# Optimization experiments

Hardware: AMD Instinct MI355X
Metric: run time of the kernel (lower is better)

The kernel has to match this reference:

```python
import jax, jax.numpy as jnp
import numpy as np

B, CIN, COUT, H, W = 8, 128, 128, 256, 256
M1, M2 = 64, 64


def setup_inputs() -> dict:
    key = jax.random.key(0)
    k1, k2 = jax.random.split(key)
    x = jax.random.normal(k1, (B, CIN, H, W), dtype=jnp.float32)
    scale = 1.0 / (CIN * COUT)
    # real-valued param, last dim 2 = (real, imag), matching torch.view_as_complex layout
    weights = scale * jax.random.uniform(k2, (CIN, COUT, M1, M2, 2), dtype=jnp.float32)
    return {"x": x, "weights": weights}


def reference(x, weights):
    Bn, C, Hn, Wn = x.shape
    m1, m2 = weights.shape[2], weights.shape[3]
    out_ch = weights.shape[1]
    w_c = weights[..., 0] + 1j * weights[..., 1]          # [i,o,m1,m2] complex
    x_ft = jnp.fft.rfft2(x, norm='ortho')                 # [B,C,H,W//2+1] complex
    # truncated complex mode mixing
    mixed = jnp.einsum('bixy,ioxy->boxy', x_ft[:, :, :m1, :m2], w_c)
    out_ft = jnp.zeros((Bn, out_ch, Hn, Wn // 2 + 1), dtype=mixed.dtype)
    out_ft = out_ft.at[:, :, :m1, :m2].set(mixed)
    return jnp.fft.irfft2(out_ft, s=(Hn, Wn), norm='ortho')  # [B,out,H,W] real
```

## Files before the change

kernel.cpp:

```cpp
#include <hip/hip_runtime.h>
#include <cstddef>


typedef __attribute__((ext_vector_type(8))) short bf16x8;
typedef __attribute__((ext_vector_type(4))) float f32x4;
typedef unsigned short u16;

static constexpr float T256 = 6.28318530717958647692f / 256.0f;
static constexpr int FB_OFF = 4096, IB_OFF = 12288, IA_OFF = 20480;

__device__ __forceinline__ u16 f2bf(float f) {
    unsigned u = __float_as_uint(f);
    return (u16)((u + 0x7FFFu + ((u >> 16) & 1u)) >> 16);
}
__device__ __forceinline__ ushort4 cvt4(const f32x4& a) {
    ushort4 o;
    o.x = f2bf(a[0]); o.y = f2bf(a[1]); o.z = f2bf(a[2]); o.w = f2bf(a[3]);
    return o;
}

__global__ __launch_bounds__(256) void gen_kernel(u16* __restrict__ tw) {
    const int t = blockIdx.x * 256 + threadIdx.x;
    const int lane = t & 63, f = t >> 6;
    const int lr = lane & 15, lg = lane >> 4;
    bf16x8 hi;
#pragma unroll
    for (int j = 0; j < 8; ++j) {
        float v = 0.0f;
        if (f < 64) {
            int nf = f >> 3, ks = f & 7;
            int col = nf * 16 + lr, k = ks * 32 + lg * 8 + j;
            int cc = (col < 64) ? col : (col - 64);
            float ss, sc; sincosf(T256 * (float)((k * cc) & 255), &ss, &sc);
            v = (col < 64) ? sc : ss;
        } else if (f < 192) {
            int fid = f - 64, nf = fid >> 4, ks = fid & 15;
            int col = nf * 16 + lr, k = ks * 32 + lg * 8 + j;
            int kx = col & 63, im = col >> 6;
            int h = k & 255, part = k >> 8;
            float ss, sc; sincosf(T256 * (float)((h * kx) & 255), &ss, &sc);
            if (im == 0) v = part ? -ss : sc;
            else         v = part ? -sc : -ss;
        } else if (f < 320) {
            int fid = f - 192, nf = fid >> 2, ks = fid & 3;
            int col = nf * 16 + lr, k = ks * 32 + lg * 8 + j;
            int h = col & 255, reim = col >> 8;
            int kx = k & 63, part = k >> 6;
            float ss, sc; sincosf(T256 * (float)((h * kx) & 255), &ss, &sc);
            if (reim == 0) v = part ? -ss : sc;
            else           v = part ?  sc :  ss;
        } else {
            int fid = f - 320, mf = fid >> 2, ks = fid & 3;
            int w = mf * 16 + lr, k = ks * 32 + lg * 8 + j;
            int ky = k & 63, part = k >> 6;
            float wt = (ky ? 2.0f : 1.0f) * (1.0f / 65536.0f);
            float ss, sc; sincosf(T256 * (float)((w * ky) & 255), &ss, &sc);
            v = part ? (-wt * ss) : (wt * sc);
        }
        hi[j] = (short)f2bf(v);
    }
    *(bf16x8*)(tw + (size_t)t * 8) = hi;
}

__global__ __launch_bounds__(256, 4) void fa_kernel(const float* __restrict__ x,
                                                    const u16* __restrict__ tw,
                                                    u16* __restrict__ Tt) {
    const int bi = blockIdx.x >> 2, hc = blockIdx.x & 3;
    const int tid = threadIdx.x;
    const int lane = tid & 63, wid = tid >> 6;
    const int lr = lane & 15, lg = lane >> 4;

    __shared__ u16 Ls[128][72];

    f32x4 acc[8] = {};
    const float* xr = x + (size_t)bi * 65536 + (size_t)(hc * 64 + wid * 16 + lr) * 256 + lg * 8;

    f32x4 xv[16];
#pragma unroll
    for (int ks = 0; ks < 8; ++ks) {
        xv[2 * ks]     = *(const f32x4*)(xr + ks * 32);
        xv[2 * ks + 1] = *(const f32x4*)(xr + ks * 32 + 4);
    }

#pragma unroll
    for (int ks = 0; ks < 8; ++ks) {
        bf16x8 ah;
#pragma unroll
        for (int j = 0; j < 4; ++j) {
            ah[j]     = (short)f2bf(xv[2 * ks][j]);
            ah[4 + j] = (short)f2bf(xv[2 * ks + 1][j]);
        }
#pragma unroll
        for (int nf = 0; nf < 8; ++nf) {
            bf16x8 bh = *(const bf16x8*)(tw + ((size_t)(nf * 8 + ks) * 64 + lane) * 8);
            acc[nf] = __builtin_amdgcn_mfma_f32_16x16x32_bf16(ah, bh, acc[nf], 0, 0, 0);
        }
    }

#pragma unroll
    for (int nf = 0; nf < 8; ++nf)
        *(ushort4*)&Ls[nf * 16 + lr][wid * 16 + lg * 4] = cvt4(acc[nf]);
    __syncthreads();

    {
        const int col = tid >> 1, half = tid & 1;
        const int ky = col & 63, cs = col >> 6;
        u16* dst = Tt + (size_t)bi * 32768 + (size_t)ky * 512 + cs * 256 + hc * 64 + half * 32;
        const u16* srcp = &Ls[col][half * 32];
#pragma unroll
        for (int q = 0; q < 4; ++q)
            *(bf16x8*)(dst + q * 8) = *(const bf16x8*)(srcp + q * 8);
    }
}

__global__ __launch_bounds__(256, 4) void fb_kernel(const u16* __restrict__ Tt,
                                                    const u16* __restrict__ tw,
                                                    float2* __restrict__ Y) {
    const int bi = blockIdx.x;
    const int tid = threadIdx.x;
    const int lane = tid & 63, wid = tid >> 6;
    const int lr = lane & 15, lg = lane >> 4;

    f32x4 acc[8] = {};
    const u16* ar = Tt + (size_t)bi * 32768 + (size_t)(wid * 16 + lr) * 512 + lg * 8;

#pragma unroll 2
    for (int ks = 0; ks < 16; ++ks) {
        bf16x8 ah = *(const bf16x8*)(ar + ks * 32);
#pragma unroll
        for (int nf = 0; nf < 8; ++nf) {
            bf16x8 bh = *(const bf16x8*)(tw + ((size_t)FB_OFF + (size_t)(nf * 16 + ks) * 64 + lane) * 8);
            acc[nf] = __builtin_amdgcn_mfma_f32_16x16x32_bf16(ah, bh, acc[nf], 0, 0, 0);
        }
    }

    __shared__ float L[64][129];
#pragma unroll
    for (int nf = 0; nf < 8; ++nf) {
        int col = nf * 16 + lr;
        int row = wid * 16 + lg * 4;
#pragma unroll
        for (int r = 0; r < 4; ++r) L[row + r][col] = acc[nf][r];
    }
    __syncthreads();
#pragma unroll
    for (int s = 0; s < 16; ++s) {
        int n = tid + s * 256;
        int ky = n & 63, kx = n >> 6;
        Y[(size_t)bi * 4096 + n] = make_float2(L[ky][kx], L[ky][64 + kx]);
    }
}

__global__ __launch_bounds__(256) void mix_kernel(const float2* Yin,
                                                  const float* __restrict__ Wg,
                                                  float2* Mx) {
    const int kx    = blockIdx.x & 63;
    const int kyo   = blockIdx.x >> 6;
    const int tid   = threadIdx.x;
    const int kxky0 = kx * 64 + kyo * 8;

    __shared__ float2 Ys[128 * 64];

#pragma unroll
    for (int s = 0; s < 32; ++s) {
        int n = tid + s * 256;
        int b = n >> 10, i = (n >> 3) & 127, j = n & 7;
        Ys[i * 64 + b * 8 + j] = Yin[(size_t)(b * 128 + i) * 4096 + kxky0 + j];
    }
    __syncthreads();

    const int o  = tid >> 1;
    const int jh = tid & 1;

    float accre[8][4] = {{0.f}}, accim[8][4] = {{0.f}};
    const float* wp = Wg + ((size_t)o * 4096 + kxky0 + jh * 4) * 2;
    const size_t istride = (size_t)128 * 4096 * 2;

#pragma unroll 2
    for (int i = 0; i < 128; ++i) {
        float4 wa = *(const float4*)(wp + (size_t)i * istride);
        float4 wb = *(const float4*)(wp + (size_t)i * istride + 4);
#pragma unroll
        for (int b = 0; b < 8; ++b) {
            float4 y01 = *(const float4*)&Ys[i * 64 + b * 8 + jh * 4];
            float4 y23 = *(const float4*)&Ys[i * 64 + b * 8 + jh * 4 + 2];
            accre[b][0] = fmaf(y01.x, wa.x, fmaf(-y01.y, wa.y, accre[b][0]));
            accim[b][0] = fmaf(y01.x, wa.y, fmaf( y01.y, wa.x, accim[b][0]));
            accre[b][1] = fmaf(y01.z, wa.z, fmaf(-y01.w, wa.w, accre[b][1]));
            accim[b][1] = fmaf(y01.z, wa.w, fmaf( y01.w, wa.z, accim[b][1]));
            accre[b][2] = fmaf(y23.x, wb.x, fmaf(-y23.y, wb.y, accre[b][2]));
            accim[b][2] = fmaf(y23.x, wb.y, fmaf( y23.y, wb.x, accim[b][2]));
            accre[b][3] = fmaf(y23.z, wb.z, fmaf(-y23.w, wb.w, accre[b][3]));
            accim[b][3] = fmaf(y23.z, wb.w, fmaf( y23.w, wb.z, accim[b][3]));
        }
    }
#pragma unroll
    for (int b = 0; b < 8; ++b) {
        float2* mo = Mx + (size_t)(b * 128 + o) * 4096 + kxky0 + jh * 4;
        *(float4*)(mo)     = make_float4(accre[b][0], accim[b][0], accre[b][1], accim[b][1]);
        *(float4*)(mo + 2) = make_float4(accre[b][2], accim[b][2], accre[b][3], accim[b][3]);
    }
}

__global__ __launch_bounds__(256, 4) void ib_kernel(const float2* __restrict__ M,
                                                    const u16* __restrict__ tw,
                                                    u16* __restrict__ Gt) {
    const int bo = blockIdx.x >> 1, reim = blockIdx.x & 1;
    const int tid = threadIdx.x;
    const int lane = tid & 63, wid = tid >> 6;
    const int lr = lane & 15, lg = lane >> 4;

    __shared__ __align__(16) char smem[256 * 72 * 2];
    u16 (*Ah)[136] = (u16(*)[136])smem;
    u16 (*Gs)[72]  = (u16(*)[72])smem;

    const float2* Mb = M + (size_t)bo * 4096;
#pragma unroll
    for (int s = 0; s < 16; ++s) {
        int n = tid + s * 256;
        float2 v = Mb[n];
        int kx = n >> 6, ky = n & 63;
        Ah[ky][kx]      = f2bf(v.x);
        Ah[ky][64 + kx] = f2bf(v.y);
    }
    __syncthreads();

    f32x4 bacc[4][4] = {};
#pragma unroll
    for (int ks = 0; ks < 4; ++ks) {
        bf16x8 bh[4];
#pragma unroll
        for (int nf = 0; nf < 4; ++nf) {
            int nf_g = reim * 16 + wid * 4 + nf;
            bh[nf] = *(const bf16x8*)(tw + ((size_t)IB_OFF + (size_t)(nf_g * 4 + ks) * 64 + lane) * 8);
        }
#pragma unroll
        for (int mf = 0; mf < 4; ++mf) {
            bf16x8 ah = *(const bf16x8*)&Ah[mf * 16 + lr][ks * 32 + lg * 8];
#pragma unroll
            for (int nf = 0; nf < 4; ++nf)
                bacc[mf][nf] = __builtin_amdgcn_mfma_f32_16x16x32_bf16(ah, bh[nf], bacc[mf][nf], 0, 0, 0);
        }
    }
    __syncthreads();

#pragma unroll
    for (int mf = 0; mf < 4; ++mf)
#pragma unroll
        for (int nf = 0; nf < 4; ++nf)
            *(ushort4*)&Gs[wid * 64 + nf * 16 + lr][mf * 16 + lg * 4] = cvt4(bacc[mf][nf]);
    __syncthreads();

    {
        const u16* srcp = &Gs[tid][0];
        u16* dst = Gt + (size_t)bo * 32768 + (size_t)tid * 128 + reim * 64;
#pragma unroll
        for (int q = 0; q < 8; ++q)
            *(bf16x8*)(dst + q * 8) = *(const bf16x8*)(srcp + q * 8);
    }
}

__global__ __launch_bounds__(256, 4) void ia_kernel(const u16* __restrict__ Gt,
                                                    const u16* __restrict__ tw,
                                                    float* __restrict__ out) {
    const int bo = blockIdx.x >> 2, hq = blockIdx.x & 3;
    const int lane = threadIdx.x & 63, wid = threadIdx.x >> 6;
    const int lr = lane & 15, lg = lane >> 4;

    f32x4 cacc[4][4] = {};
    const u16* gb = Gt + (size_t)bo * 32768 + (size_t)(hq * 64) * 128;

#pragma unroll
    for (int ks = 0; ks < 4; ++ks) {
        bf16x8 ah[4];
#pragma unroll
        for (int mf = 0; mf < 4; ++mf) {
            int mf_g = wid * 4 + mf;
            ah[mf] = *(const bf16x8*)(tw + ((size_t)IA_OFF + (size_t)(mf_g * 4 + ks) * 64 + lane) * 8);
        }
#pragma unroll
        for (int nf = 0; nf < 4; ++nf) {
            bf16x8 bh = *(const bf16x8*)(gb + (size_t)(nf * 16 + lr) * 128 + ks * 32 + lg * 8);
#pragma unroll
            for (int mf = 0; mf < 4; ++mf)
                cacc[mf][nf] = __builtin_amdgcn_mfma_f32_16x16x32_bf16(ah[mf], bh, cacc[mf][nf], 0, 0, 0);
        }
    }
#pragma unroll
    for (int mf = 0; mf < 4; ++mf)
#pragma unroll
        for (int nf = 0; nf < 4; ++nf) {
            int w0 = wid * 64 + mf * 16 + lg * 4;
            int h  = hq * 64 + nf * 16 + lr;
            *(f32x4*)(out + (size_t)bo * 65536 + (size_t)h * 256 + w0) = cacc[mf][nf];
        }
}

extern "C" void kernel_launch(void* const* d_in, const int* in_sizes, int n_in,
                              void* d_out, int out_size, void* d_ws, size_t ws_size,
                              hipStream_t stream) {
    (void)in_sizes; (void)n_in; (void)out_size; (void)ws_size;
    const float* x  = (const float*)d_in[0];
    const float* wg = (const float*)d_in[1];
    float* outp = (float*)d_out;

    u16*    tw = (u16*)d_ws;
    float2* Y  = (float2*)((char*)d_ws + 1048576);
    u16*    Tt = (u16*)((char*)d_ws + 1048576 + 33554432);
    u16*    Gt = (u16*)((char*)d_ws + 1048576 + 33554432 + 67108864);

    gen_kernel<<<96, 256, 0, stream>>>(tw);
    fa_kernel<<<4096, 256, 0, stream>>>(x, tw, Tt);
    fb_kernel<<<1024, 256, 0, stream>>>(Tt, tw, Y);
    mix_kernel<<<512, 256, 0, stream>>>(Y, wg, Y);
    ib_kernel<<<2048, 256, 0, stream>>>(Y, tw, Gt);
    ia_kernel<<<4096, 256, 0, stream>>>(Gt, tw, outp);
}
```

Baseline: 425.2 us.

## Fuse inverse column and row DFT stages into one kernel via shared memory

Merges the two inverse-transform kernels into a single kernel. Each block now computes its 64-row slice of the intermediate G in shared memory and immediately applies the second DFT GEMM to it, so the bf16 Gt round trip through global memory goes away, along with one launch. The cost is that each of the four h-quarter blocks per (b,o) reloads and reconverts the full 64x64 mode tile M. Shared memory per block also grows.

New measurement: 371.5 us, median of 2. 12.6% less time.

```diff
diff --git a/kernel.cpp b/kernel.cpp
--- a/kernel.cpp
+++ b/kernel.cpp
@@ -202,17 +202,16 @@
     }
 }
 
-__global__ __launch_bounds__(256, 4) void ib_kernel(const float2* __restrict__ M,
-                                                    const u16* __restrict__ tw,
-                                                    u16* __restrict__ Gt) {
-    const int bo = blockIdx.x >> 1, reim = blockIdx.x & 1;
+__global__ __launch_bounds__(256, 4) void inv_kernel(const float2* __restrict__ M,
+                                                     const u16* __restrict__ tw,
+                                                     float* __restrict__ out) {
+    const int bo = blockIdx.x >> 2, hq = blockIdx.x & 3;
     const int tid = threadIdx.x;
     const int lane = tid & 63, wid = tid >> 6;
     const int lr = lane & 15, lg = lane >> 4;
 
-    __shared__ __align__(16) char smem[256 * 72 * 2];
-    u16 (*Ah)[136] = (u16(*)[136])smem;
-    u16 (*Gs)[72]  = (u16(*)[72])smem;
+    __shared__ u16 Ah[64][136];
+    __shared__ u16 Gh[64][136];
 
     const float2* Mb = M + (size_t)bo * 4096;
 #pragma unroll
@@ -225,75 +224,64 @@
     }
     __syncthreads();
 
-    f32x4 bacc[4][4] = {};
-#pragma unroll
-    for (int ks = 0; ks < 4; ++ks) {
-        bf16x8 bh[4];
-#pragma unroll
-        for (int nf = 0; nf < 4; ++nf) {
-            int nf_g = reim * 16 + wid * 4 + nf;
-            bh[nf] = *(const bf16x8*)(tw + ((size_t)IB_OFF + (size_t)(nf_g * 4 + ks) * 64 + lane) * 8);
-        }
-#pragma unroll
-        for (int mf = 0; mf < 4; ++mf) {
-            bf16x8 ah = *(const bf16x8*)&Ah[mf * 16 + lr][ks * 32 + lg * 8];
-#pragma unroll
-            for (int nf = 0; nf < 4; ++nf)
-                bacc[mf][nf] = __builtin_amdgcn_mfma_f32_16x16x32_bf16(ah, bh[nf], bacc[mf][nf], 0, 0, 0);
-        }
-    }
-    __syncthreads();
-
-#pragma unroll
-    for (int mf = 0; mf < 4; ++mf)
-#pragma unroll
-        for (int nf = 0; nf < 4; ++nf)
-            *(ushort4*)&Gs[wid * 64 + nf * 16 + lr][mf * 16 + lg * 4] = cvt4(bacc[mf][nf]);
-    __syncthreads();
-
     {
-        const u16* srcp = &Gs[tid][0];
-        u16* dst = Gt + (size_t)bo * 32768 + (size_t)tid * 128 + reim * 64;
-#pragma unroll
-        for (int q = 0; q < 8; ++q)
-            *(bf16x8*)(dst + q * 8) = *(const bf16x8*)(srcp + q * 8);
-    }
-}
-
-__global__ __launch_bounds__(256, 4) void ia_kernel(const u16* __restrict__ Gt,
-                                                    const u16* __restrict__ tw,
-                                                    float* __restrict__ out) {
-    const int bo = blockIdx.x >> 2, hq = blockIdx.x & 3;
-    const int lane = threadIdx.x & 63, wid = threadIdx.x >> 6;
-    const int lr = lane & 15, lg = lane >> 4;
-
-    f32x4 cacc[4][4] = {};
-    const u16* gb = Gt + (size_t)bo * 32768 + (size_t)(hq * 64) * 128;
-
-#pragma unroll
-    for (int ks = 0; ks < 4; ++ks) {
-        bf16x8 ah[4];
-#pragma unroll
-        for (int mf = 0; mf < 4; ++mf) {
-            int mf_g = wid * 4 + mf;
-            ah[mf] = *(const bf16x8*)(tw + ((size_t)IA_OFF + (size_t)(mf_g * 4 + ks) * 64 + lane) * 8);
-        }
-#pragma unroll
-        for (int nf = 0; nf < 4; ++nf) {
-            bf16x8 bh = *(const bf16x8*)(gb + (size_t)(nf * 16 + lr) * 128 + ks * 32 + lg * 8);
-#pragma unroll
-            for (int mf = 0; mf < 4; ++mf)
-                cacc[mf][nf] = __builtin_amdgcn_mfma_f32_16x16x32_bf16(ah[mf], bh, cacc[mf][nf], 0, 0, 0);
-        }
-    }
-#pragma unroll
-    for (int mf = 0; mf < 4; ++mf)
-#pragma unroll
-        for (int nf = 0; nf < 4; ++nf) {
-            int w0 = wid * 64 + mf * 16 + lg * 4;
-            int h  = hq * 64 + nf * 16 + lr;
-            *(f32x4*)(out + (size_t)bo * 65536 + (size_t)h * 256 + w0) = cacc[mf][nf];
-        }
+        const int reim = wid >> 1, csub = wid & 1;
+        f32x4 bacc[4][2] = {};
+#pragma unroll
+        for (int ks = 0; ks < 4; ++ks) {
+            bf16x8 bh[2];
+#pragma unroll
+            for (int nf = 0; nf < 2; ++nf) {
+                int nf_g = reim * 16 + hq * 4 + csub * 2 + nf;
+                bh[nf] = *(const bf16x8*)(tw + ((size_t)IB_OFF + (size_t)(nf_g * 4 + ks) * 64 + lane) * 8);
+            }
+#pragma unroll
+            for (int mf = 0; mf < 4; ++mf) {
+                bf16x8 ah = *(const bf16x8*)&Ah[mf * 16 + lr][ks * 32 + lg * 8];
+#pragma unroll
+                for (int nf = 0; nf < 2; ++nf)
+                    bacc[mf][nf] = __builtin_amdgcn_mfma_f32_16x16x32_bf16(ah, bh[nf], bacc[mf][nf], 0, 0, 0);
+            }
+        }
+        __syncthreads();
+#pragma unroll
+        for (int mf = 0; mf < 4; ++mf)
+#pragma unroll
+            for (int nf = 0; nf < 2; ++nf) {
+                int hloc = csub * 32 + nf * 16 + lr;
+                int kk   = reim * 64 + mf * 16 + lg * 4;
+                *(ushort4*)&Gh[hloc][kk] = cvt4(bacc[mf][nf]);
+            }
+    }
+    __syncthreads();
+
+    {
+        f32x4 cacc[4][4] = {};
+#pragma unroll
+        for (int ks = 0; ks < 4; ++ks) {
+            bf16x8 ah[4];
+#pragma unroll
+            for (int mf = 0; mf < 4; ++mf) {
+                int mf_g = wid * 4 + mf;
+                ah[mf] = *(const bf16x8*)(tw + ((size_t)IA_OFF + (size_t)(mf_g * 4 + ks) * 64 + lane) * 8);
+            }
+#pragma unroll
+            for (int nf = 0; nf < 4; ++nf) {
+                bf16x8 bh = *(const bf16x8*)&Gh[nf * 16 + lr][ks * 32 + lg * 8];
+#pragma unroll
+                for (int mf = 0; mf < 4; ++mf)
+                    cacc[mf][nf] = __builtin_amdgcn_mfma_f32_16x16x32_bf16(ah[mf], bh, cacc[mf][nf], 0, 0, 0);
+            }
+        }
+#pragma unroll
+        for (int mf = 0; mf < 4; ++mf)
+#pragma unroll
+            for (int nf = 0; nf < 4; ++nf) {
+                int w0 = wid * 64 + mf * 16 + lg * 4;
+                int h  = hq * 64 + nf * 16 + lr;
+                *(f32x4*)(out + (size_t)bo * 65536 + (size_t)h * 256 + w0) = cacc[mf][nf];
+            }
+    }
 }
 
 extern "C" void kernel_launch(void* const* d_in, const int* in_sizes, int n_in,
@@ -307,12 +295,10 @@
     u16*    tw = (u16*)d_ws;
     float2* Y  = (float2*)((char*)d_ws + 1048576);
     u16*    Tt = (u16*)((char*)d_ws + 1048576 + 33554432);
-    u16*    Gt = (u16*)((char*)d_ws + 1048576 + 33554432 + 67108864);
 
     gen_kernel<<<96, 256, 0, stream>>>(tw);
     fa_kernel<<<4096, 256, 0, stream>>>(x, tw, Tt);
     fb_kernel<<<1024, 256, 0, stream>>>(Tt, tw, Y);
     mix_kernel<<<512, 256, 0, stream>>>(Y, wg, Y);
-    ib_kernel<<<2048, 256, 0, stream>>>(Y, tw, Gt);
-    ia_kernel<<<4096, 256, 0, stream>>>(Gt, tw, outp);
-}
+    inv_kernel<<<4096, 256, 0, stream>>>(Y, tw, outp);
+}
```
